# Optimization experiments

Measured on AMD Instinct MI355X. Metric: run time of the kernel, lower is better.

## Reference

```python
import jax, jax.numpy as jnp
import numpy as np

N, C, C2 = 768, 384, 128
H, PQK, PV, CQK, CV = 12, 4, 8, 16, 16
EPS_DIST = 1e-8


def quat_to_rot(q):
    q = q / jnp.linalg.norm(q, axis=-1, keepdims=True)
    w, x, y, z = q[..., 0], q[..., 1], q[..., 2], q[..., 3]
    r0 = jnp.stack([1 - 2 * (y * y + z * z), 2 * (x * y - w * z), 2 * (x * z + w * y)], -1)
    r1 = jnp.stack([2 * (x * y + w * z), 1 - 2 * (x * x + z * z), 2 * (y * z - w * x)], -1)
    r2 = jnp.stack([2 * (x * z - w * y), 2 * (y * z + w * x), 1 - 2 * (x * x + y * y)], -1)
    return jnp.stack([r0, r1, r2], -2)


def layer_norm(x, scale, bias):
    mu = jnp.mean(x, -1, keepdims=True)
    var = jnp.var(x, -1, keepdims=True)
    return (x - mu) * jax.lax.rsqrt(var + 1e-5) * scale + bias


def project_points(x, w, b, rot, trans, p):
    # Linear -> [N,H,3p], split into x/y/z local coords, apply rigid to get global points
    pl = (x @ w + b).reshape(x.shape[0], H, 3 * p)
    loc = jnp.stack(jnp.split(pl, 3, axis=-1), -1)                        # [N,H,p,3]
    return jnp.einsum('nij,nhpj->nhpi', rot, loc) + trans[:, None, None, :]


def setup_inputs() -> dict:
    ks = iter(jax.random.split(jax.random.key(0), 64))
    rn = lambda shape, s: jax.random.normal(next(ks), shape, jnp.float32) * s
    w = lambda shape: rn(shape, 0.02)
    return {
        'inputs_1d': rn([N, C], 1.0),
        'inputs_2d': rn([N, N, C2], 1.0),
        'mask': jnp.ones([N, 1], jnp.float32),
        'rot': quat_to_rot(jax.random.normal(next(ks), [N, 4], jnp.float32)),
        'trans': rn([N, 3], 10.0),
        'w_q_point': w([C, H * 3 * PQK]), 'b_q_point': jnp.zeros([H * 3 * PQK], jnp.float32),
        'w_k_point': w([C, H * 3 * PQK]), 'b_k_point': jnp.zeros([H * 3 * PQK], jnp.float32),
        'w_v_point': w([C, H * 3 * PV]), 'b_v_point': jnp.zeros([H * 3 * PV], jnp.float32),
        'w_q_scalar': w([C, H * CQK]), 'w_k_scalar': w([C, H * CQK]), 'w_v_scalar': w([C, H * CV]),
        'tpw': jnp.full([H], np.log(np.e - 1.0), jnp.float32),
        'w_2d': w([C2, H]), 'b_2d': jnp.zeros([H], jnp.float32),
        'w_out': w([H * CV + 4 * H * PV + H * C2, C]), 'b_out': jnp.zeros([C], jnp.float32),
        'ln1_s': jnp.ones([C], jnp.float32), 'ln1_b': jnp.zeros([C], jnp.float32),
        'w_t1': w([C, C]), 'b_t1': jnp.zeros([C], jnp.float32),
        'w_t2': w([C, C]), 'b_t2': jnp.zeros([C], jnp.float32),
        'w_t3': w([C, C]), 'b_t3': jnp.zeros([C], jnp.float32),
        'ln2_s': jnp.ones([C], jnp.float32), 'ln2_b': jnp.zeros([C], jnp.float32),
        'w_quat': w([C, 6]), 'b_quat': jnp.zeros([6], jnp.float32),
    }


def reference(inputs_1d, inputs_2d, mask, rot, trans,
              w_q_point, b_q_point, w_k_point, b_k_point, w_v_point, b_v_point,
              w_q_scalar, w_k_scalar, w_v_scalar, tpw, w_2d, b_2d, w_out, b_out,
              ln1_s, ln1_b, w_t1, b_t1, w_t2, b_t2, w_t3, b_t3, ln2_s, ln2_b,
              w_quat, b_quat):
    n = inputs_1d.shape[0]
    # ---- Invariant Point Attention ----
    point_w = np.sqrt(2.0 / (9.0 * max(PQK, 1))) * jax.nn.softplus(tpw)   # [H]
    qg = project_points(inputs_1d, w_q_point, b_q_point, rot, trans, PQK)  # [N,H,PQK,3]
    kg = project_points(inputs_1d, w_k_point, b_k_point, rot, trans, PQK)
    # sum_p |q-k|^2 expanded as |q|^2 + |k|^2 - 2 q.k to avoid the [N,N,H,P,3] tensor
    qn = jnp.sum(qg * qg, axis=(-1, -2))                                   # [N,H]
    kn = jnp.sum(kg * kg, axis=(-1, -2))
    cross = jnp.einsum('qhpd,khpd->qkh', qg, kg)
    dist2 = qn[:, None] + kn[None] - 2.0 * cross                           # [N,N,H]
    logits = -0.5 * point_w * dist2
    qs = (inputs_1d @ w_q_scalar).reshape(n, H, CQK) * np.sqrt(1.0 / CQK)
    ksc = (inputs_1d @ w_k_scalar).reshape(n, H, CQK)
    logits += jnp.einsum('qhc,khc->qkh', qs, ksc)
    logits += inputs_2d @ w_2d + b_2d                                      # [N,N,H]
    mask_2d = mask * jnp.swapaxes(mask, -1, -2)                            # [N,N]
    logits -= 1e5 * (1.0 - mask_2d[..., None])
    logits *= np.sqrt(1.0 / 3.0)
    attn = jax.nn.softmax(logits, axis=-2)                                 # softmax over keys
    vs = (inputs_1d @ w_v_scalar).reshape(n, H, CV)
    res_scalar = jnp.einsum('qkh,khc->qhc', attn, vs).reshape(n, -1)
    vg = project_points(inputs_1d, w_v_point, b_v_point, rot, trans, PV)   # [N,H,PV,3]
    rp_g = jnp.einsum('qkh,khpd->qhpd', attn, vg)
    rp_l = jnp.einsum('qdi,qhpd->qhpi', rot, rp_g - trans[:, None, None, :])  # rigid^-1
    norms = jnp.sqrt(jnp.maximum(jnp.sum(rp_l * rp_l, -1), EPS_DIST ** 2))
    res_2d = jnp.einsum('qkh,qkc->qhc', attn, inputs_2d).reshape(n, -1)
    final = jnp.concatenate([
        res_scalar,
        rp_l[..., 0].reshape(n, -1), rp_l[..., 1].reshape(n, -1), rp_l[..., 2].reshape(n, -1),
        norms.reshape(n, -1), res_2d], axis=-1)
    attn_out = final @ w_out + b_out
    # ---- residual + LayerNorm + transition MLP ----
    act = layer_norm(inputs_1d + attn_out, ln1_s, ln1_b)
    x = jax.nn.relu(act @ w_t1 + b_t1)
    x = jax.nn.relu(x @ w_t2 + b_t2)
    x = x @ w_t3 + b_t3
    act = layer_norm(act + x, ln2_s, ln2_b)
    # ---- rigid (quaternion) update: quat = (1, a, b, c), compose with input rigid ----
    v6 = act @ w_quat + b_quat
    quat = jnp.concatenate([jnp.ones_like(v6[:, :1]), v6[:, :3]], -1)
    rot_u = quat_to_rot(quat)
    rot_new = jnp.einsum('nij,njk->nik', rot, rot_u)
    trans_new = jnp.einsum('nij,nj->ni', rot, v6[:, 3:]) + trans
    return jnp.concatenate([act, rot_new.reshape(n, 9), trans_new], axis=-1)
```

## Files before the change

kernel.cpp:

```cpp
#include <hip/hip_runtime.h>


typedef unsigned short bfu;
typedef unsigned int u32;

__device__ __forceinline__ float bf2f(bfu u) {
    return __uint_as_float(((u32)u) << 16);
}
__device__ __forceinline__ bfu f2bf(float f) {
    u32 x = __float_as_uint(f);
    u32 r = x + 0x7fffu + ((x >> 16) & 1u);
    return (bfu)(r >> 16);
}
__device__ __forceinline__ float bflo(u32 u) { return __uint_as_float(u << 16); }
__device__ __forceinline__ float bfhi(u32 u) { return __uint_as_float(u & 0xffff0000u); }

#define OFF_PL      0u
#define OFF_FQ      1769472u
#define OFF_GK      2949120u
#define OFF_VST     4128768u
#define OFF_VGT     4423680u
#define OFF_LOGITS  4866048u
#define OFF_FINAL   33177600u
#define OFF_ATTNOUT 36421632u
#define OFF_ACT     37011456u
#define OFF_X1      37601280u
#define OFF_X2      38191104u
#define OFF_WCAT    38780928u
#define OFF_BCAT    39665664u
#define OFF_CONV    39667968u
#define OFF_FLAG    43684288u

#define CONV_TOTAL 2008158

struct P30 { const void* p[30]; };

static __device__ const int kEnd[30] = {
    294912, 295680, 302592, 304896, 360192, 360336, 415632, 415776,
    526368, 526656, 600384, 674112, 747840, 747852, 749388, 749400,
    1560408, 1560792, 1561176, 1561560, 1709016, 1709400, 1856856, 1857240,
    2004696, 2005080, 2005464, 2005848, 2008152, 2008158
};

__global__ __launch_bounds__(256) void k_convert(P30 ps, bfu* __restrict__ conv,
                                                 u32* __restrict__ flags) {
    u32 pm = *(const u32*)ps.p[1];
    u32 pp = *(const u32*)ps.p[18];
    u32 fA = (pm == 0x3F800000u) ? 1u : 0u;
    u32 fB = (pp == 0x3F800000u) ? 1u : 0u;
    int idx = blockIdx.x * 256 + threadIdx.x;
    if (idx == 0) { flags[0] = fA; flags[1] = fA & fB; }
    if (idx >= CONV_TOTAL) return;
    int t = 0;
    while (idx >= kEnd[t]) ++t;
    int local = idx - (t ? kEnd[t - 1] : 0);
    u32 f = (t < 4) ? fA : fB;
    float v = f ? ((const float*)ps.p[t])[local]
                : bf2f(((const bfu*)ps.p[t])[local]);
    conv[idx] = f2bf(v);
}

__global__ __launch_bounds__(256) void k_concat(
    const bfu* __restrict__ wqs, const bfu* __restrict__ wks, const bfu* __restrict__ wvs,
    const bfu* __restrict__ wqp, const bfu* __restrict__ bqp,
    const bfu* __restrict__ wkp, const bfu* __restrict__ bkp,
    const bfu* __restrict__ wvp, const bfu* __restrict__ bvp,
    bfu* __restrict__ wcat, bfu* __restrict__ bcat) {
    int idx = blockIdx.x * 256 + threadIdx.x;
    if (idx < 384 * 1152) {
        int row = idx / 1152, col = idx - row * 1152;
        bfu v;
        if      (col < 192) v = wqs[row * 192 + col];
        else if (col < 384) v = wks[row * 192 + col - 192];
        else if (col < 576) v = wvs[row * 192 + col - 384];
        else if (col < 720) v = wqp[row * 144 + col - 576];
        else if (col < 864) v = wkp[row * 144 + col - 720];
        else                v = wvp[row * 288 + col - 864];
        wcat[idx] = v;
    } else if (idx < 384 * 1152 + 1152) {
        int col = idx - 384 * 1152;
        bfu v;
        if      (col < 576) v = 0;
        else if (col < 720) v = bqp[col - 576];
        else if (col < 864) v = bkp[col - 720];
        else                v = bvp[col - 864];
        bcat[col] = v;
    }
}

template <int RELU>
__global__ __launch_bounds__(256) void k_gemm(
    const bfu* __restrict__ A, const bfu* __restrict__ W, const bfu* __restrict__ bias,
    bfu* __restrict__ out, int K, int M) {
    __shared__ float As[32][34];
    __shared__ float Ws[32][34];
    int t = threadIdx.x;
    int c0 = blockIdx.x * 32, r0 = blockIdx.y * 32;
    int tr = t >> 4, tc = t & 15;
    float a00 = 0, a01 = 0, a10 = 0, a11 = 0;
    int nch = K >> 5;
    for (int ch = 0; ch < nch; ++ch) {
        int kc = ch * 32;
#pragma unroll
        for (int i = 0; i < 4; ++i) {
            int idx = t + i * 256;
            int r = idx >> 5, c = idx & 31;
            As[c][r] = bf2f(A[(size_t)(r0 + r) * K + kc + c]);
        }
#pragma unroll
        for (int i = 0; i < 4; ++i) {
            int idx = t + i * 256;
            int r = idx >> 5, c = idx & 31;
            Ws[r][c] = bf2f(W[(size_t)(kc + r) * M + c0 + c]);
        }
        __syncthreads();
#pragma unroll
        for (int kk = 0; kk < 32; ++kk) {
            float x0 = As[kk][2 * tr], x1 = As[kk][2 * tr + 1];
            float w0 = Ws[kk][2 * tc], w1 = Ws[kk][2 * tc + 1];
            a00 += x0 * w0; a01 += x0 * w1;
            a10 += x1 * w0; a11 += x1 * w1;
        }
        __syncthreads();
    }
    float b0 = bf2f(bias[c0 + 2 * tc]), b1 = bf2f(bias[c0 + 2 * tc + 1]);
    float v00 = a00 + b0, v01 = a01 + b1, v10 = a10 + b0, v11 = a11 + b1;
    if (RELU) {
        v00 = fmaxf(v00, 0.f); v01 = fmaxf(v01, 0.f);
        v10 = fmaxf(v10, 0.f); v11 = fmaxf(v11, 0.f);
    }
    u32 p0 = (u32)f2bf(v00) | ((u32)f2bf(v01) << 16);
    u32 p1 = (u32)f2bf(v10) | ((u32)f2bf(v11) << 16);
    *(u32*)&out[(size_t)(r0 + 2 * tr) * M + c0 + 2 * tc] = p0;
    *(u32*)&out[(size_t)(r0 + 2 * tr + 1) * M + c0 + 2 * tc] = p1;
}

__global__ __launch_bounds__(64) void k_rigid(
    const bfu* __restrict__ pl, const bfu* __restrict__ rot, const bfu* __restrict__ trans,
    const bfu* __restrict__ tpw, const bfu* __restrict__ b2d,
    float* __restrict__ fq, float* __restrict__ gk,
    bfu* __restrict__ vsT, bfu* __restrict__ vgT) {
    int n = blockIdx.x, t = threadIdx.x;
    __shared__ float pls[1152];
    __shared__ float qgs[144], kgs[144];
    __shared__ float rs[9], ts3[3], pws[12], qns[12], kns[12];
    for (int i = t; i < 1152; i += 64) pls[i] = bf2f(pl[(size_t)n * 1152 + i]);
    if (t < 9)  rs[t] = bf2f(rot[n * 9 + t]);
    if (t < 3)  ts3[t] = bf2f(trans[n * 3 + t]);
    if (t < 12) pws[t] = 0.23570226039551584f * log1pf(expf(bf2f(tpw[t])));
    __syncthreads();
    for (int idx = t; idx < 144; idx += 64) {
        int h = idx / 12, r = idx - h * 12, p = r / 3, i = r - p * 3;
        float q0 = pls[576 + h * 12 + p], q1 = pls[576 + h * 12 + 4 + p], q2 = pls[576 + h * 12 + 8 + p];
        qgs[idx] = rs[i * 3 + 0] * q0 + rs[i * 3 + 1] * q1 + rs[i * 3 + 2] * q2 + ts3[i];
        float k0 = pls[720 + h * 12 + p], k1 = pls[720 + h * 12 + 4 + p], k2 = pls[720 + h * 12 + 8 + p];
        kgs[idx] = rs[i * 3 + 0] * k0 + rs[i * 3 + 1] * k1 + rs[i * 3 + 2] * k2 + ts3[i];
    }
    for (int idx = t; idx < 288; idx += 64) {
        int h = idx / 24, r = idx - h * 24, p = r / 3, i = r - p * 3;
        float v0 = pls[864 + h * 24 + p], v1 = pls[864 + h * 24 + 8 + p], v2 = pls[864 + h * 24 + 16 + p];
        float v = rs[i * 3 + 0] * v0 + rs[i * 3 + 1] * v1 + rs[i * 3 + 2] * v2 + ts3[i];
        vgT[(size_t)idx * 768 + n] = f2bf(v);
    }
    __syncthreads();
    if (t < 12) {
        float s = 0;
        for (int j = 0; j < 12; ++j) s += qgs[t * 12 + j] * qgs[t * 12 + j];
        qns[t] = s;
        s = 0;
        for (int j = 0; j < 12; ++j) s += kgs[t * 12 + j] * kgs[t * 12 + j];
        kns[t] = s;
    }
    __syncthreads();
    for (int idx = t; idx < 12 * 32; idx += 64) {
        int h = idx >> 5, j = idx & 31;
        float fv, gv;
        if (j < 16)      { fv = 0.25f * pls[h * 16 + j];      gv = pls[192 + h * 16 + j]; }
        else if (j < 28) { fv = qgs[h * 12 + j - 16];         gv = pws[h] * kgs[h * 12 + j - 16]; }
        else if (j == 28){ fv = -0.5f * pws[h] * qns[h];      gv = 1.0f; }
        else if (j == 29){ fv = 1.0f;                          gv = -0.5f * pws[h] * kns[h]; }
        else if (j == 30){ fv = bf2f(b2d[h]);                  gv = 1.0f; }
        else             { fv = 0.0f;                          gv = 0.0f; }
        fq[((size_t)n * 12 + h) * 32 + j] = fv;
        gk[((size_t)n * 12 + h) * 32 + j] = gv;
    }
    for (int idx = t; idx < 192; idx += 64)
        vsT[(size_t)idx * 768 + n] = f2bf(pls[384 + idx]);
}

__global__ __launch_bounds__(256) void k2a(
    const float* __restrict__ fq, const float* __restrict__ gk, float* __restrict__ logits) {
    int t = threadIdx.x;
    int k0 = blockIdx.x * 64, q0 = blockIdx.y * 64, h = blockIdx.z;
    __shared__ float Fs[64][33], Gs[64][33];
#pragma unroll
    for (int i = 0; i < 8; ++i) {
        int idx = t + i * 256;
        int r = idx >> 5, c = idx & 31;
        Fs[r][c] = fq[((size_t)(q0 + r) * 12 + h) * 32 + c];
        Gs[r][c] = gk[((size_t)(k0 + r) * 12 + h) * 32 + c];
    }
    __syncthreads();
    int tq = t >> 4, tk = t & 15;
    float acc[4][4] = {};
#pragma unroll
    for (int kk = 0; kk < 32; ++kk) {
        float f0 = Fs[tq * 4 + 0][kk], f1 = Fs[tq * 4 + 1][kk];
        float f2 = Fs[tq * 4 + 2][kk], f3 = Fs[tq * 4 + 3][kk];
        float g0 = Gs[tk * 4 + 0][kk], g1 = Gs[tk * 4 + 1][kk];
        float g2 = Gs[tk * 4 + 2][kk], g3 = Gs[tk * 4 + 3][kk];
        acc[0][0] += f0 * g0; acc[0][1] += f0 * g1; acc[0][2] += f0 * g2; acc[0][3] += f0 * g3;
        acc[1][0] += f1 * g0; acc[1][1] += f1 * g1; acc[1][2] += f1 * g2; acc[1][3] += f1 * g3;
        acc[2][0] += f2 * g0; acc[2][1] += f2 * g1; acc[2][2] += f2 * g2; acc[2][3] += f2 * g3;
        acc[3][0] += f3 * g0; acc[3][1] += f3 * g1; acc[3][2] += f3 * g2; acc[3][3] += f3 * g3;
    }
#pragma unroll
    for (int i = 0; i < 4; ++i) {
        float4 v = make_float4(acc[i][0], acc[i][1], acc[i][2], acc[i][3]);
        *(float4*)&logits[((size_t)h * 768 + q0 + tq * 4 + i) * 768 + k0 + tk * 4] = v;
    }
}

__global__ __launch_bounds__(256) void k2b(
    const void* __restrict__ in2dv, const bfu* __restrict__ w2d,
    const bfu* __restrict__ mask, float* __restrict__ logits,
    const u32* __restrict__ flags) {
    int t = threadIdx.x;
    int q = blockIdx.y, k = blockIdx.x * 256 + t;
    bool f32m = flags[0] != 0u;
    __shared__ __align__(16) float w2ds[12 * 128];
    for (int i = t; i < 1536; i += 256) {
        int cc = i / 12, hh2 = i - cc * 12;
        w2ds[hh2 * 128 + cc] = bf2f(w2d[i]);
    }
    __syncthreads();
    float acc[12] = {};
    size_t base = ((size_t)q * 768 + k) * 128;
    if (f32m) {
        const float4* p = (const float4*)((const float*)in2dv + base);
#pragma unroll 8
        for (int cb = 0; cb < 32; ++cb) {
            float4 u = p[cb];
#pragma unroll
            for (int h = 0; h < 12; ++h) {
                float4 w = *(const float4*)&w2ds[h * 128 + cb * 4];
                acc[h] += u.x * w.x + u.y * w.y + u.z * w.z + u.w * w.w;
            }
        }
    } else {
        const uint2* p = (const uint2*)((const bfu*)in2dv + base);
#pragma unroll 8
        for (int cb = 0; cb < 32; ++cb) {
            uint2 u = p[cb];
            float f0 = bflo(u.x), f1 = bfhi(u.x), f2 = bflo(u.y), f3 = bfhi(u.y);
#pragma unroll
            for (int h = 0; h < 12; ++h) {
                float4 w = *(const float4*)&w2ds[h * 128 + cb * 4];
                acc[h] += f0 * w.x + f1 * w.y + f2 * w.z + f3 * w.w;
            }
        }
    }
    float mq = bf2f(mask[q]), mk = bf2f(mask[k]);
    float mterm = 100000.0f * (1.0f - mq * mk);
#pragma unroll
    for (int h = 0; h < 12; ++h) {
        size_t idx = ((size_t)h * 768 + q) * 768 + k;
        logits[idx] = (logits[idx] + acc[h] - mterm) * 0.5773502691896258f;
    }
}

__global__ __launch_bounds__(256) void k3(
    const float* __restrict__ logits, const void* __restrict__ in2dv,
    const bfu* __restrict__ vsT, const bfu* __restrict__ vgT,
    const bfu* __restrict__ rot, const bfu* __restrict__ trans,
    bfu* __restrict__ finalb, const u32* __restrict__ flags) {
    int q = blockIdx.x, t = threadIdx.x;
    bool f32m = flags[0] != 0u;
    __shared__ __align__(16) float attT[12 * 776];
    __shared__ __align__(16) bfu tile[64 * 128];
    __shared__ float rpg[288];
    __shared__ float rots[9], trs[3];

    for (int h = 0; h < 12; ++h)
        for (int k = t; k < 768; k += 256)
            attT[h * 776 + k] = logits[((size_t)h * 768 + q) * 768 + k];
    __syncthreads();

    if (t < 192) {
        int h = t >> 4, g = t & 15;
        float m = -1e30f;
        for (int i = 0; i < 48; ++i) m = fmaxf(m, attT[h * 776 + g + i * 16]);
#pragma unroll
        for (int off = 1; off < 16; off <<= 1) m = fmaxf(m, __shfl_xor(m, off));
        float s = 0.f;
        for (int i = 0; i < 48; ++i) {
            float v = __expf(attT[h * 776 + g + i * 16] - m);
            attT[h * 776 + g + i * 16] = v;
            s += v;
        }
#pragma unroll
        for (int off = 1; off < 16; off <<= 1) s += __shfl_xor(s, off);
        float rinv = 1.0f / s;
        for (int i = 0; i < 48; ++i) attT[h * 776 + g + i * 16] *= rinv;
    }
    if (t >= 192 && t < 201) rots[t - 192] = bf2f(rot[q * 9 + t - 192]);
    if (t >= 201 && t < 204) trs[t - 201] = bf2f(trans[q * 3 + t - 201]);
    __syncthreads();

    int cp = t & 63, h0 = t >> 6;
    float p00 = 0, p01 = 0, p10 = 0, p11 = 0, p20 = 0, p21 = 0;
    for (int ch = 0; ch < 12; ++ch) {
#pragma unroll
        for (int i = 0; i < 4; ++i) {
            int idx = t + i * 256;
            int r = idx >> 4, g = idx & 15;
            if (f32m) {
                const float* src = (const float*)in2dv +
                    ((size_t)(q * 768 + ch * 64 + r)) * 128 + g * 8;
                float4 a = *(const float4*)src;
                float4 b = *(const float4*)(src + 4);
                uint4 w;
                w.x = (u32)f2bf(a.x) | ((u32)f2bf(a.y) << 16);
                w.y = (u32)f2bf(a.z) | ((u32)f2bf(a.w) << 16);
                w.z = (u32)f2bf(b.x) | ((u32)f2bf(b.y) << 16);
                w.w = (u32)f2bf(b.z) | ((u32)f2bf(b.w) << 16);
                ((uint4*)tile)[idx] = w;
            } else {
                ((uint4*)tile)[idx] = *(const uint4*)((const bfu*)in2dv +
                    ((size_t)(q * 768 + ch * 64 + r)) * 128 + g * 8);
            }
        }
        __syncthreads();
        const u32* tp = (const u32*)tile;
        const float4* a0p = (const float4*)&attT[(h0 + 0) * 776 + ch * 64];
        const float4* a1p = (const float4*)&attT[(h0 + 4) * 776 + ch * 64];
        const float4* a2p = (const float4*)&attT[(h0 + 8) * 776 + ch * 64];
#pragma unroll 4
        for (int k4 = 0; k4 < 16; ++k4) {
            float4 a0 = a0p[k4], a1 = a1p[k4], a2 = a2p[k4];
            float a0v[4] = {a0.x, a0.y, a0.z, a0.w};
            float a1v[4] = {a1.x, a1.y, a1.z, a1.w};
            float a2v[4] = {a2.x, a2.y, a2.z, a2.w};
#pragma unroll
            for (int u = 0; u < 4; ++u) {
                u32 uu = tp[(k4 * 4 + u) * 64 + cp];
                float lo = bflo(uu), hi = bfhi(uu);
                p00 += a0v[u] * lo; p01 += a0v[u] * hi;
                p10 += a1v[u] * lo; p11 += a1v[u] * hi;
                p20 += a2v[u] * lo; p21 += a2v[u] * hi;
            }
        }
        __syncthreads();
    }
    {
        bfu* fb = finalb + (size_t)q * 2112 + 576;
        *(u32*)&fb[(h0 + 0) * 128 + 2 * cp] = (u32)f2bf(p00) | ((u32)f2bf(p01) << 16);
        *(u32*)&fb[(h0 + 4) * 128 + 2 * cp] = (u32)f2bf(p10) | ((u32)f2bf(p11) << 16);
        *(u32*)&fb[(h0 + 8) * 128 + 2 * cp] = (u32)f2bf(p20) | ((u32)f2bf(p21) << 16);
    }

    if (t < 120) {
        int h = t / 10, oi = t - h * 10;
        const bfu* rp[4];
#pragma unroll
        for (int j = 0; j < 4; ++j) {
            int o = oi * 4 + j;
            rp[j] = (o < 16) ? (vsT + (size_t)(h * 16 + o) * 768)
                             : (vgT + (size_t)(h * 24 + o - 16) * 768);
        }
        float acc[4] = {};
        for (int kb = 0; kb < 96; ++kb) {
            int k8 = kb * 8;
            float4 aL = *(const float4*)&attT[h * 776 + k8];
            float4 aH = *(const float4*)&attT[h * 776 + k8 + 4];
#pragma unroll
            for (int j = 0; j < 4; ++j) {
                uint4 u = *(const uint4*)(rp[j] + k8);
                acc[j] += aL.x * bflo(u.x) + aL.y * bfhi(u.x)
                        + aL.z * bflo(u.y) + aL.w * bfhi(u.y)
                        + aH.x * bflo(u.z) + aH.y * bfhi(u.z)
                        + aH.z * bflo(u.w) + aH.w * bfhi(u.w);
            }
        }
#pragma unroll
        for (int j = 0; j < 4; ++j) {
            int o = oi * 4 + j;
            if (o < 16) finalb[(size_t)q * 2112 + h * 16 + o] = f2bf(acc[j]);
            else rpg[h * 24 + o - 16] = acc[j];
        }
    }
    __syncthreads();

    if (t < 96) {
        int h = t >> 3, p = t & 7;
        float v0 = rpg[h * 24 + p * 3 + 0] - trs[0];
        float v1 = rpg[h * 24 + p * 3 + 1] - trs[1];
        float v2 = rpg[h * 24 + p * 3 + 2] - trs[2];
        float r0 = rots[0] * v0 + rots[3] * v1 + rots[6] * v2;
        float r1 = rots[1] * v0 + rots[4] * v1 + rots[7] * v2;
        float r2 = rots[2] * v0 + rots[5] * v1 + rots[8] * v2;
        float nn = sqrtf(fmaxf(r0 * r0 + r1 * r1 + r2 * r2, 1e-16f));
        size_t fb = (size_t)q * 2112;
        finalb[fb + 192 + h * 8 + p] = f2bf(r0);
        finalb[fb + 288 + h * 8 + p] = f2bf(r1);
        finalb[fb + 384 + h * 8 + p] = f2bf(r2);
        finalb[fb + 480 + h * 8 + p] = f2bf(nn);
    }
}

__global__ __launch_bounds__(128) void k_ln(
    const bfu* __restrict__ a, const bfu* __restrict__ b,
    const bfu* __restrict__ sc, const bfu* __restrict__ bi,
    bfu* __restrict__ outb, void* __restrict__ outf, const u32* __restrict__ flags) {
    int r = blockIdx.x, t = threadIdx.x;
    __shared__ float red[2][2];
    float x[3];
    float s = 0.f, ss = 0.f;
#pragma unroll
    for (int i = 0; i < 3; ++i) {
        int c = t + i * 128;
        float v = bf2f(a[(size_t)r * 384 + c]) + bf2f(b[(size_t)r * 384 + c]);
        x[i] = v; s += v; ss += v * v;
    }
#pragma unroll
    for (int off = 1; off < 64; off <<= 1) { s += __shfl_xor(s, off); ss += __shfl_xor(ss, off); }
    int w = t >> 6;
    if ((t & 63) == 0) { red[w][0] = s; red[w][1] = ss; }
    __syncthreads();
    s = red[0][0] + red[1][0];
    ss = red[0][1] + red[1][1];
    float mu = s * (1.0f / 384.0f);
    float var = ss * (1.0f / 384.0f) - mu * mu;
    float rstd = rsqrtf(var + 1e-5f);
    bool f32o = flags[1] != 0u;
#pragma unroll
    for (int i = 0; i < 3; ++i) {
        int c = t + i * 128;
        float v = (x[i] - mu) * rstd * bf2f(sc[c]) + bf2f(bi[c]);
        outb[(size_t)r * 384 + c] = f2bf(v);
        if (outf) {
            if (f32o) ((float*)outf)[(size_t)r * 396 + c] = v;
            else      ((bfu*)outf)[(size_t)r * 396 + c] = f2bf(v);
        }
    }
}

__global__ __launch_bounds__(64) void k_quat(
    const bfu* __restrict__ act2,
    const bfu* __restrict__ rot, const bfu* __restrict__ trans,
    const bfu* __restrict__ wq, const bfu* __restrict__ bq,
    void* __restrict__ doutv, const u32* __restrict__ flags) {
    int r = blockIdx.x, t = threadIdx.x;
    float acc[6] = {};
    for (int i = 0; i < 6; ++i) {
        int k = t + i * 64;
        float xv = bf2f(act2[(size_t)r * 384 + k]);
#pragma unroll
        for (int o = 0; o < 6; ++o) acc[o] += xv * bf2f(wq[k * 6 + o]);
    }
#pragma unroll
    for (int o = 0; o < 6; ++o) {
#pragma unroll
        for (int off = 1; off < 64; off <<= 1) acc[o] += __shfl_xor(acc[o], off);
    }
    if (t == 0) {
        bool f32o = flags[1] != 0u;
        float v[6];
        for (int o = 0; o < 6; ++o) v[o] = acc[o] + bf2f(bq[o]);
        float w_ = 1.0f, x_ = v[0], y_ = v[1], z_ = v[2];
        float inv = rsqrtf(w_ * w_ + x_ * x_ + y_ * y_ + z_ * z_);
        w_ *= inv; x_ *= inv; y_ *= inv; z_ *= inv;
        float U[9];
        U[0] = 1 - 2 * (y_ * y_ + z_ * z_); U[1] = 2 * (x_ * y_ - w_ * z_); U[2] = 2 * (x_ * z_ + w_ * y_);
        U[3] = 2 * (x_ * y_ + w_ * z_); U[4] = 1 - 2 * (x_ * x_ + z_ * z_); U[5] = 2 * (y_ * z_ - w_ * x_);
        U[6] = 2 * (x_ * z_ - w_ * y_); U[7] = 2 * (y_ * z_ + w_ * x_); U[8] = 1 - 2 * (x_ * x_ + y_ * y_);
        float R[9];
        for (int i = 0; i < 9; ++i) R[i] = bf2f(rot[r * 9 + i]);
        for (int i = 0; i < 3; ++i)
            for (int j = 0; j < 3; ++j) {
                float sum = R[i * 3] * U[j] + R[i * 3 + 1] * U[3 + j] + R[i * 3 + 2] * U[6 + j];
                if (f32o) ((float*)doutv)[(size_t)r * 396 + 384 + i * 3 + j] = sum;
                else      ((bfu*)doutv)[(size_t)r * 396 + 384 + i * 3 + j] = f2bf(sum);
            }
        for (int i = 0; i < 3; ++i) {
            float sum = R[i * 3] * v[3] + R[i * 3 + 1] * v[4] + R[i * 3 + 2] * v[5] + bf2f(trans[r * 3 + i]);
            if (f32o) ((float*)doutv)[(size_t)r * 396 + 393 + i] = sum;
            else      ((bfu*)doutv)[(size_t)r * 396 + 393 + i] = f2bf(sum);
        }
    }
}

extern "C" void kernel_launch(void* const* d_in, const int* in_sizes, int n_in,
                              void* d_out, int out_size, void* d_ws, size_t ws_size,
                              hipStream_t stream) {
    (void)in_sizes; (void)n_in; (void)out_size; (void)ws_size;

    char* ws = (char*)d_ws;
    bfu* pl      = (bfu*)(ws + OFF_PL);
    float* fq    = (float*)(ws + OFF_FQ);
    float* gk    = (float*)(ws + OFF_GK);
    bfu* vsT     = (bfu*)(ws + OFF_VST);
    bfu* vgT     = (bfu*)(ws + OFF_VGT);
    float* logit = (float*)(ws + OFF_LOGITS);
    bfu* finalb  = (bfu*)(ws + OFF_FINAL);
    bfu* attnout = (bfu*)(ws + OFF_ATTNOUT);
    bfu* act     = (bfu*)(ws + OFF_ACT);
    bfu* x1      = (bfu*)(ws + OFF_X1);
    bfu* x2      = (bfu*)(ws + OFF_X2);
    bfu* act2    = x2;
    bfu* wcat    = (bfu*)(ws + OFF_WCAT);
    bfu* bcat    = (bfu*)(ws + OFF_BCAT);
    bfu* conv    = (bfu*)(ws + OFF_CONV);
    u32* flags   = (u32*)(ws + OFF_FLAG);

    static const int offs[30] = {
        0, 294912, 295680, 302592, 304896, 360192, 360336, 415632, 415776,
        526368, 526656, 600384, 674112, 747840, 747852, 749388, 749400,
        1560408, 1560792, 1561176, 1561560, 1709016, 1709400, 1856856, 1857240,
        2004696, 2005080, 2005464, 2005848, 2008152
    };
    const bfu* c_in1d = conv + offs[0];
    const bfu* c_mask = conv + offs[1];
    const bfu* c_rot  = conv + offs[2];
    const bfu* c_trns = conv + offs[3];
    const bfu* c_wqp  = conv + offs[4];
    const bfu* c_bqp  = conv + offs[5];
    const bfu* c_wkp  = conv + offs[6];
    const bfu* c_bkp  = conv + offs[7];
    const bfu* c_wvp  = conv + offs[8];
    const bfu* c_bvp  = conv + offs[9];
    const bfu* c_wqs  = conv + offs[10];
    const bfu* c_wks  = conv + offs[11];
    const bfu* c_wvs  = conv + offs[12];
    const bfu* c_tpw  = conv + offs[13];
    const bfu* c_w2d  = conv + offs[14];
    const bfu* c_b2d  = conv + offs[15];
    const bfu* c_wout = conv + offs[16];
    const bfu* c_bout = conv + offs[17];
    const bfu* c_ln1s = conv + offs[18];
    const bfu* c_ln1b = conv + offs[19];
    const bfu* c_wt1  = conv + offs[20];
    const bfu* c_bt1  = conv + offs[21];
    const bfu* c_wt2  = conv + offs[22];
    const bfu* c_bt2  = conv + offs[23];
    const bfu* c_wt3  = conv + offs[24];
    const bfu* c_bt3  = conv + offs[25];
    const bfu* c_ln2s = conv + offs[26];
    const bfu* c_ln2b = conv + offs[27];
    const bfu* c_wqt  = conv + offs[28];
    const bfu* c_bqt  = conv + offs[29];

    P30 ps;
    ps.p[0] = d_in[0];
    for (int i = 1; i < 30; ++i) ps.p[i] = d_in[i + 1];
    const void* in2d = d_in[1];

    k_convert<<<(CONV_TOTAL + 255) / 256, 256, 0, stream>>>(ps, conv, flags);
    k_concat<<<1733, 256, 0, stream>>>(c_wqs, c_wks, c_wvs, c_wqp, c_bqp, c_wkp, c_bkp,
                                       c_wvp, c_bvp, wcat, bcat);
    k_gemm<0><<<dim3(36, 24), 256, 0, stream>>>(c_in1d, wcat, bcat, pl, 384, 1152);
    k_rigid<<<768, 64, 0, stream>>>(pl, c_rot, c_trns, c_tpw, c_b2d, fq, gk, vsT, vgT);
    k2a<<<dim3(12, 12, 12), 256, 0, stream>>>(fq, gk, logit);
    k2b<<<dim3(3, 768), 256, 0, stream>>>(in2d, c_w2d, c_mask, logit, flags);
    k3<<<768, 256, 0, stream>>>(logit, in2d, vsT, vgT, c_rot, c_trns, finalb, flags);
    k_gemm<0><<<dim3(12, 24), 256, 0, stream>>>(finalb, c_wout, c_bout, attnout, 2112, 384);
    k_ln<<<768, 128, 0, stream>>>(c_in1d, attnout, c_ln1s, c_ln1b, act, nullptr, flags);
    k_gemm<1><<<dim3(12, 24), 256, 0, stream>>>(act, c_wt1, c_bt1, x1, 384, 384);
    k_gemm<1><<<dim3(12, 24), 256, 0, stream>>>(x1, c_wt2, c_bt2, x2, 384, 384);
    k_gemm<0><<<dim3(12, 24), 256, 0, stream>>>(x2, c_wt3, c_bt3, x1, 384, 384);
    k_ln<<<768, 128, 0, stream>>>(act, x1, c_ln2s, c_ln2b, act2, d_out, flags);
    k_quat<<<768, 64, 0, stream>>>(act2, c_rot, c_trns, c_wqt, c_bqt, d_out, flags);
}
```

Before: 955.8 us.

## Fuse logits, pair bias and softmax per query; retile GEMMs to 64x64

Replaces the separate logits GEMM, pair-bias pass and softmax with one per-query kernel. It computes the point and scalar logits from a transposed key-feature buffer, adds the 2D bias, applies softmax in shared memory and writes normalized attention. The aggregation kernel now streams inputs_2d directly without a staged shared tile and splits value work across more threads. The GEMMs move to 64x64 tiles with 4x4 register blocking and packed loads. Together this removes a logits round trip and several launches, at the cost of strided per-key global reads in the fused kernel and lower GEMM block counts.

```diff
diff --git a/kernel.cpp b/kernel.cpp
--- a/kernel.cpp
+++ b/kernel.cpp
@@ -17,10 +17,10 @@
 
 #define OFF_PL      0u
 #define OFF_FQ      1769472u
-#define OFF_GK      2949120u
+#define OFF_GKT     2949120u
 #define OFF_VST     4128768u
 #define OFF_VGT     4423680u
-#define OFF_LOGITS  4866048u
+#define OFF_ATTN    4866048u
 #define OFF_FINAL   33177600u
 #define OFF_ATTNOUT 36421632u
 #define OFF_ACT     37011456u
@@ -89,56 +89,65 @@
 }
 
 template <int RELU>
-__global__ __launch_bounds__(256) void k_gemm(
+__global__ __launch_bounds__(256) void k_gemm64(
     const bfu* __restrict__ A, const bfu* __restrict__ W, const bfu* __restrict__ bias,
     bfu* __restrict__ out, int K, int M) {
-    __shared__ float As[32][34];
-    __shared__ float Ws[32][34];
+    __shared__ float As[32][69];
+    __shared__ float Ws[32][69];
     int t = threadIdx.x;
-    int c0 = blockIdx.x * 32, r0 = blockIdx.y * 32;
+    int c0 = blockIdx.x * 64, r0 = blockIdx.y * 64;
     int tr = t >> 4, tc = t & 15;
-    float a00 = 0, a01 = 0, a10 = 0, a11 = 0;
-    int nch = K >> 5;
-    for (int ch = 0; ch < nch; ++ch) {
-        int kc = ch * 32;
+    float acc[4][4] = {};
+    for (int kc = 0; kc < K; kc += 32) {
 #pragma unroll
         for (int i = 0; i < 4; ++i) {
             int idx = t + i * 256;
-            int r = idx >> 5, c = idx & 31;
-            As[c][r] = bf2f(A[(size_t)(r0 + r) * K + kc + c]);
+            int r = idx >> 4, c2 = idx & 15;
+            u32 u = *(const u32*)&A[(size_t)(r0 + r) * K + kc + 2 * c2];
+            As[2 * c2][r] = bflo(u); As[2 * c2 + 1][r] = bfhi(u);
         }
 #pragma unroll
         for (int i = 0; i < 4; ++i) {
             int idx = t + i * 256;
-            int r = idx >> 5, c = idx & 31;
-            Ws[r][c] = bf2f(W[(size_t)(kc + r) * M + c0 + c]);
+            int r = idx >> 5, c2 = idx & 31;
+            u32 u = *(const u32*)&W[(size_t)(kc + r) * M + c0 + 2 * c2];
+            Ws[r][2 * c2] = bflo(u); Ws[r][2 * c2 + 1] = bfhi(u);
         }
         __syncthreads();
 #pragma unroll
         for (int kk = 0; kk < 32; ++kk) {
-            float x0 = As[kk][2 * tr], x1 = As[kk][2 * tr + 1];
-            float w0 = Ws[kk][2 * tc], w1 = Ws[kk][2 * tc + 1];
-            a00 += x0 * w0; a01 += x0 * w1;
-            a10 += x1 * w0; a11 += x1 * w1;
+            float x[4], w[4];
+#pragma unroll
+            for (int j = 0; j < 4; ++j) { x[j] = As[kk][4 * tr + j]; w[j] = Ws[kk][4 * tc + j]; }
+#pragma unroll
+            for (int a = 0; a < 4; ++a)
+#pragma unroll
+                for (int b = 0; b < 4; ++b) acc[a][b] += x[a] * w[b];
         }
         __syncthreads();
     }
-    float b0 = bf2f(bias[c0 + 2 * tc]), b1 = bf2f(bias[c0 + 2 * tc + 1]);
-    float v00 = a00 + b0, v01 = a01 + b1, v10 = a10 + b0, v11 = a11 + b1;
-    if (RELU) {
-        v00 = fmaxf(v00, 0.f); v01 = fmaxf(v01, 0.f);
-        v10 = fmaxf(v10, 0.f); v11 = fmaxf(v11, 0.f);
-    }
-    u32 p0 = (u32)f2bf(v00) | ((u32)f2bf(v01) << 16);
-    u32 p1 = (u32)f2bf(v10) | ((u32)f2bf(v11) << 16);
-    *(u32*)&out[(size_t)(r0 + 2 * tr) * M + c0 + 2 * tc] = p0;
-    *(u32*)&out[(size_t)(r0 + 2 * tr + 1) * M + c0 + 2 * tc] = p1;
+    float bv[4];
+#pragma unroll
+    for (int b = 0; b < 4; ++b) bv[b] = bf2f(bias[c0 + 4 * tc + b]);
+#pragma unroll
+    for (int a = 0; a < 4; ++a) {
+        float v[4];
+#pragma unroll
+        for (int b = 0; b < 4; ++b) {
+            v[b] = acc[a][b] + bv[b];
+            if (RELU) v[b] = fmaxf(v[b], 0.f);
+        }
+        uint2 pk;
+        pk.x = (u32)f2bf(v[0]) | ((u32)f2bf(v[1]) << 16);
+        pk.y = (u32)f2bf(v[2]) | ((u32)f2bf(v[3]) << 16);
+        *(uint2*)&out[(size_t)(r0 + 4 * tr + a) * M + c0 + 4 * tc] = pk;
+    }
 }
 
 __global__ __launch_bounds__(64) void k_rigid(
     const bfu* __restrict__ pl, const bfu* __restrict__ rot, const bfu* __restrict__ trans,
     const bfu* __restrict__ tpw, const bfu* __restrict__ b2d,
-    float* __restrict__ fq, float* __restrict__ gk,
+    float* __restrict__ fq, float* __restrict__ gkT,
     bfu* __restrict__ vsT, bfu* __restrict__ vgT) {
     int n = blockIdx.x, t = threadIdx.x;
     __shared__ float pls[1152];
@@ -181,176 +190,141 @@
         else if (j == 29){ fv = 1.0f;                          gv = -0.5f * pws[h] * kns[h]; }
         else if (j == 30){ fv = bf2f(b2d[h]);                  gv = 1.0f; }
         else             { fv = 0.0f;                          gv = 0.0f; }
-        fq[((size_t)n * 12 + h) * 32 + j] = fv;
-        gk[((size_t)n * 12 + h) * 32 + j] = gv;
+        fq[(size_t)n * 384 + idx] = fv;
+        gkT[(size_t)idx * 768 + n] = gv;
     }
     for (int idx = t; idx < 192; idx += 64)
         vsT[(size_t)idx * 768 + n] = f2bf(pls[384 + idx]);
 }
 
-__global__ __launch_bounds__(256) void k2a(
-    const float* __restrict__ fq, const float* __restrict__ gk, float* __restrict__ logits) {
-    int t = threadIdx.x;
-    int k0 = blockIdx.x * 64, q0 = blockIdx.y * 64, h = blockIdx.z;
-    __shared__ float Fs[64][33], Gs[64][33];
-#pragma unroll
-    for (int i = 0; i < 8; ++i) {
-        int idx = t + i * 256;
-        int r = idx >> 5, c = idx & 31;
-        Fs[r][c] = fq[((size_t)(q0 + r) * 12 + h) * 32 + c];
-        Gs[r][c] = gk[((size_t)(k0 + r) * 12 + h) * 32 + c];
-    }
-    __syncthreads();
-    int tq = t >> 4, tk = t & 15;
-    float acc[4][4] = {};
-#pragma unroll
-    for (int kk = 0; kk < 32; ++kk) {
-        float f0 = Fs[tq * 4 + 0][kk], f1 = Fs[tq * 4 + 1][kk];
-        float f2 = Fs[tq * 4 + 2][kk], f3 = Fs[tq * 4 + 3][kk];
-        float g0 = Gs[tk * 4 + 0][kk], g1 = Gs[tk * 4 + 1][kk];
-        float g2 = Gs[tk * 4 + 2][kk], g3 = Gs[tk * 4 + 3][kk];
-        acc[0][0] += f0 * g0; acc[0][1] += f0 * g1; acc[0][2] += f0 * g2; acc[0][3] += f0 * g3;
-        acc[1][0] += f1 * g0; acc[1][1] += f1 * g1; acc[1][2] += f1 * g2; acc[1][3] += f1 * g3;
-        acc[2][0] += f2 * g0; acc[2][1] += f2 * g1; acc[2][2] += f2 * g2; acc[2][3] += f2 * g3;
-        acc[3][0] += f3 * g0; acc[3][1] += f3 * g1; acc[3][2] += f3 * g2; acc[3][3] += f3 * g3;
-    }
-#pragma unroll
-    for (int i = 0; i < 4; ++i) {
-        float4 v = make_float4(acc[i][0], acc[i][1], acc[i][2], acc[i][3]);
-        *(float4*)&logits[((size_t)h * 768 + q0 + tq * 4 + i) * 768 + k0 + tk * 4] = v;
-    }
-}
-
-__global__ __launch_bounds__(256) void k2b(
+__global__ __launch_bounds__(256) void k_fused(
+    const float* __restrict__ fq, const float* __restrict__ gkT,
     const void* __restrict__ in2dv, const bfu* __restrict__ w2d,
-    const bfu* __restrict__ mask, float* __restrict__ logits,
+    const bfu* __restrict__ mask, float* __restrict__ attn,
     const u32* __restrict__ flags) {
-    int t = threadIdx.x;
-    int q = blockIdx.y, k = blockIdx.x * 256 + t;
+    int q = blockIdx.x, t = threadIdx.x;
     bool f32m = flags[0] != 0u;
+    __shared__ float lg[12 * 776];
     __shared__ __align__(16) float w2ds[12 * 128];
+    __shared__ __align__(16) float fqs[384];
     for (int i = t; i < 1536; i += 256) {
-        int cc = i / 12, hh2 = i - cc * 12;
-        w2ds[hh2 * 128 + cc] = bf2f(w2d[i]);
-    }
-    __syncthreads();
-    float acc[12] = {};
-    size_t base = ((size_t)q * 768 + k) * 128;
-    if (f32m) {
-        const float4* p = (const float4*)((const float*)in2dv + base);
+        int cc = i / 12, hh = i - cc * 12;
+        w2ds[hh * 128 + cc] = bf2f(w2d[i]);
+    }
+    for (int i = t; i < 384; i += 256) fqs[i] = fq[(size_t)q * 384 + i];
+    float mq = bf2f(mask[q]);
+    __syncthreads();
+
+    for (int ch = 0; ch < 3; ++ch) {
+        int k = ch * 256 + t;
+        float acc[12] = {};
+        size_t base = ((size_t)q * 768 + k) * 128;
+        if (f32m) {
+            const float4* p = (const float4*)((const float*)in2dv + base);
 #pragma unroll 8
-        for (int cb = 0; cb < 32; ++cb) {
-            float4 u = p[cb];
-#pragma unroll
-            for (int h = 0; h < 12; ++h) {
-                float4 w = *(const float4*)&w2ds[h * 128 + cb * 4];
-                acc[h] += u.x * w.x + u.y * w.y + u.z * w.z + u.w * w.w;
+            for (int cb = 0; cb < 32; ++cb) {
+                float4 u = p[cb];
+#pragma unroll
+                for (int h = 0; h < 12; ++h) {
+                    float4 w = *(const float4*)&w2ds[h * 128 + cb * 4];
+                    acc[h] += u.x * w.x + u.y * w.y + u.z * w.z + u.w * w.w;
+                }
             }
-        }
-    } else {
-        const uint2* p = (const uint2*)((const bfu*)in2dv + base);
+        } else {
+            const uint2* p = (const uint2*)((const bfu*)in2dv + base);
 #pragma unroll 8
-        for (int cb = 0; cb < 32; ++cb) {
-            uint2 u = p[cb];
-            float f0 = bflo(u.x), f1 = bfhi(u.x), f2 = bflo(u.y), f3 = bfhi(u.y);
-#pragma unroll
-            for (int h = 0; h < 12; ++h) {
-                float4 w = *(const float4*)&w2ds[h * 128 + cb * 4];
-                acc[h] += f0 * w.x + f1 * w.y + f2 * w.z + f3 * w.w;
+            for (int cb = 0; cb < 32; ++cb) {
+                uint2 u = p[cb];
+                float f0 = bflo(u.x), f1 = bfhi(u.x), f2 = bflo(u.y), f3 = bfhi(u.y);
+#pragma unroll
+                for (int h = 0; h < 12; ++h) {
+                    float4 w = *(const float4*)&w2ds[h * 128 + cb * 4];
+                    acc[h] += f0 * w.x + f1 * w.y + f2 * w.z + f3 * w.w;
+                }
             }
         }
-    }
-    float mq = bf2f(mask[q]), mk = bf2f(mask[k]);
-    float mterm = 100000.0f * (1.0f - mq * mk);
-#pragma unroll
-    for (int h = 0; h < 12; ++h) {
-        size_t idx = ((size_t)h * 768 + q) * 768 + k;
-        logits[idx] = (logits[idx] + acc[h] - mterm) * 0.5773502691896258f;
-    }
-}
-
-__global__ __launch_bounds__(256) void k3(
-    const float* __restrict__ logits, const void* __restrict__ in2dv,
+        float mk = bf2f(mask[k]);
+        float mterm = 100000.0f * (1.0f - mq * mk);
+#pragma unroll 1
+        for (int h = 0; h < 12; ++h) {
+            float s = 0.f;
+            const float* g = gkT + (size_t)(h * 32) * 768 + k;
+            const float* f = fqs + h * 32;
+#pragma unroll 8
+            for (int c = 0; c < 32; ++c) s += g[(size_t)c * 768] * f[c];
+            lg[h * 776 + k] = (s + acc[h] - mterm) * 0.5773502691896258f;
+        }
+    }
+    __syncthreads();
+
+    if (t < 192) {
+        int h = t >> 4, g = t & 15;
+        float m = -1e30f;
+        for (int i = 0; i < 48; ++i) m = fmaxf(m, lg[h * 776 + g + i * 16]);
+#pragma unroll
+        for (int off = 1; off < 16; off <<= 1) m = fmaxf(m, __shfl_xor(m, off));
+        float s = 0.f;
+        for (int i = 0; i < 48; ++i) {
+            float v = __expf(lg[h * 776 + g + i * 16] - m);
+            lg[h * 776 + g + i * 16] = v;
+            s += v;
+        }
+#pragma unroll
+        for (int off = 1; off < 16; off <<= 1) s += __shfl_xor(s, off);
+        float rinv = 1.0f / s;
+        for (int i = 0; i < 48; ++i) lg[h * 776 + g + i * 16] *= rinv;
+    }
+    __syncthreads();
+    for (int h = 0; h < 12; ++h)
+        for (int k = t; k < 768; k += 256)
+            attn[(size_t)q * 9216 + h * 768 + k] = lg[h * 776 + k];
+}
+
+__global__ __launch_bounds__(256) void k3b(
+    const float* __restrict__ attn, const void* __restrict__ in2dv,
     const bfu* __restrict__ vsT, const bfu* __restrict__ vgT,
     const bfu* __restrict__ rot, const bfu* __restrict__ trans,
     bfu* __restrict__ finalb, const u32* __restrict__ flags) {
     int q = blockIdx.x, t = threadIdx.x;
     bool f32m = flags[0] != 0u;
-    __shared__ __align__(16) float attT[12 * 776];
-    __shared__ __align__(16) bfu tile[64 * 128];
+    __shared__ __align__(16) float lgs[12 * 776];
     __shared__ float rpg[288];
     __shared__ float rots[9], trs[3];
 
     for (int h = 0; h < 12; ++h)
         for (int k = t; k < 768; k += 256)
-            attT[h * 776 + k] = logits[((size_t)h * 768 + q) * 768 + k];
-    __syncthreads();
-
-    if (t < 192) {
-        int h = t >> 4, g = t & 15;
-        float m = -1e30f;
-        for (int i = 0; i < 48; ++i) m = fmaxf(m, attT[h * 776 + g + i * 16]);
-#pragma unroll
-        for (int off = 1; off < 16; off <<= 1) m = fmaxf(m, __shfl_xor(m, off));
-        float s = 0.f;
-        for (int i = 0; i < 48; ++i) {
-            float v = __expf(attT[h * 776 + g + i * 16] - m);
-            attT[h * 776 + g + i * 16] = v;
-            s += v;
-        }
-#pragma unroll
-        for (int off = 1; off < 16; off <<= 1) s += __shfl_xor(s, off);
-        float rinv = 1.0f / s;
-        for (int i = 0; i < 48; ++i) attT[h * 776 + g + i * 16] *= rinv;
-    }
-    if (t >= 192 && t < 201) rots[t - 192] = bf2f(rot[q * 9 + t - 192]);
-    if (t >= 201 && t < 204) trs[t - 201] = bf2f(trans[q * 3 + t - 201]);
+            lgs[h * 776 + k] = attn[(size_t)q * 9216 + h * 768 + k];
+    if (t < 9)  rots[t] = bf2f(rot[q * 9 + t]);
+    if (t >= 16 && t < 19) trs[t - 16] = bf2f(trans[q * 3 + t - 16]);
     __syncthreads();
 
     int cp = t & 63, h0 = t >> 6;
     float p00 = 0, p01 = 0, p10 = 0, p11 = 0, p20 = 0, p21 = 0;
-    for (int ch = 0; ch < 12; ++ch) {
-#pragma unroll
-        for (int i = 0; i < 4; ++i) {
-            int idx = t + i * 256;
-            int r = idx >> 4, g = idx & 15;
-            if (f32m) {
-                const float* src = (const float*)in2dv +
-                    ((size_t)(q * 768 + ch * 64 + r)) * 128 + g * 8;
-                float4 a = *(const float4*)src;
-                float4 b = *(const float4*)(src + 4);
-                uint4 w;
-                w.x = (u32)f2bf(a.x) | ((u32)f2bf(a.y) << 16);
-                w.y = (u32)f2bf(a.z) | ((u32)f2bf(a.w) << 16);
-                w.z = (u32)f2bf(b.x) | ((u32)f2bf(b.y) << 16);
-                w.w = (u32)f2bf(b.z) | ((u32)f2bf(b.w) << 16);
-                ((uint4*)tile)[idx] = w;
-            } else {
-                ((uint4*)tile)[idx] = *(const uint4*)((const bfu*)in2dv +
-                    ((size_t)(q * 768 + ch * 64 + r)) * 128 + g * 8);
-            }
-        }
-        __syncthreads();
-        const u32* tp = (const u32*)tile;
-        const float4* a0p = (const float4*)&attT[(h0 + 0) * 776 + ch * 64];
-        const float4* a1p = (const float4*)&attT[(h0 + 4) * 776 + ch * 64];
-        const float4* a2p = (const float4*)&attT[(h0 + 8) * 776 + ch * 64];
+    if (f32m) {
+        const float2* p2 = (const float2*)((const float*)in2dv + (size_t)q * 98304) + cp;
 #pragma unroll 4
-        for (int k4 = 0; k4 < 16; ++k4) {
-            float4 a0 = a0p[k4], a1 = a1p[k4], a2 = a2p[k4];
-            float a0v[4] = {a0.x, a0.y, a0.z, a0.w};
-            float a1v[4] = {a1.x, a1.y, a1.z, a1.w};
-            float a2v[4] = {a2.x, a2.y, a2.z, a2.w};
-#pragma unroll
-            for (int u = 0; u < 4; ++u) {
-                u32 uu = tp[(k4 * 4 + u) * 64 + cp];
-                float lo = bflo(uu), hi = bfhi(uu);
-                p00 += a0v[u] * lo; p01 += a0v[u] * hi;
-                p10 += a1v[u] * lo; p11 += a1v[u] * hi;
-                p20 += a2v[u] * lo; p21 += a2v[u] * hi;
-            }
-        }
-        __syncthreads();
+        for (int k = 0; k < 768; ++k) {
+            float2 v = p2[(size_t)k * 64];
+            float a0 = lgs[(h0 + 0) * 776 + k];
+            float a1 = lgs[(h0 + 4) * 776 + k];
+            float a2 = lgs[(h0 + 8) * 776 + k];
+            p00 += a0 * v.x; p01 += a0 * v.y;
+            p10 += a1 * v.x; p11 += a1 * v.y;
+            p20 += a2 * v.x; p21 += a2 * v.y;
+        }
+    } else {
+        const u32* pu = (const u32*)in2dv + (size_t)q * 49152 + cp;
+#pragma unroll 4
+        for (int k = 0; k < 768; ++k) {
+            u32 u = pu[(size_t)k * 64];
+            float vx = bflo(u), vy = bfhi(u);
+            float a0 = lgs[(h0 + 0) * 776 + k];
+            float a1 = lgs[(h0 + 4) * 776 + k];
+            float a2 = lgs[(h0 + 8) * 776 + k];
+            p00 += a0 * vx; p01 += a0 * vy;
+            p10 += a1 * vx; p11 += a1 * vy;
+            p20 += a2 * vx; p21 += a2 * vy;
+        }
     }
     {
         bfu* fb = finalb + (size_t)q * 2112 + 576;
@@ -359,35 +333,33 @@
         *(u32*)&fb[(h0 + 8) * 128 + 2 * cp] = (u32)f2bf(p20) | ((u32)f2bf(p21) << 16);
     }
 
-    if (t < 120) {
-        int h = t / 10, oi = t - h * 10;
-        const bfu* rp[4];
-#pragma unroll
-        for (int j = 0; j < 4; ++j) {
-            int o = oi * 4 + j;
-            rp[j] = (o < 16) ? (vsT + (size_t)(h * 16 + o) * 768)
-                             : (vgT + (size_t)(h * 24 + o - 16) * 768);
-        }
-        float acc[4] = {};
+    if (t < 240) {
+        int o0 = 2 * t;
+        int h = o0 / 40, r0 = o0 - h * 40, r1 = r0 + 1;
+        const bfu* rowA = (r0 < 16) ? (vsT + (size_t)(h * 16 + r0) * 768)
+                                    : (vgT + (size_t)(h * 24 + r0 - 16) * 768);
+        const bfu* rowB = (r1 < 16) ? (vsT + (size_t)(h * 16 + r1) * 768)
+                                    : (vgT + (size_t)(h * 24 + r1 - 16) * 768);
+        float aA = 0.f, aB = 0.f;
         for (int kb = 0; kb < 96; ++kb) {
             int k8 = kb * 8;
-            float4 aL = *(const float4*)&attT[h * 776 + k8];
-            float4 aH = *(const float4*)&attT[h * 776 + k8 + 4];
-#pragma unroll
-            for (int j = 0; j < 4; ++j) {
-                uint4 u = *(const uint4*)(rp[j] + k8);
-                acc[j] += aL.x * bflo(u.x) + aL.y * bfhi(u.x)
-                        + aL.z * bflo(u.y) + aL.w * bfhi(u.y)
-                        + aH.x * bflo(u.z) + aH.y * bfhi(u.z)
-                        + aH.z * bflo(u.w) + aH.w * bfhi(u.w);
-            }
-        }
-#pragma unroll
-        for (int j = 0; j < 4; ++j) {
-            int o = oi * 4 + j;
-            if (o < 16) finalb[(size_t)q * 2112 + h * 16 + o] = f2bf(acc[j]);
-            else rpg[h * 24 + o - 16] = acc[j];
-        }
+            float4 aL = *(const float4*)&lgs[h * 776 + k8];
+            float4 aH = *(const float4*)&lgs[h * 776 + k8 + 4];
+            uint4 uA = *(const uint4*)(rowA + k8);
+            uint4 uB = *(const uint4*)(rowB + k8);
+            aA += aL.x * bflo(uA.x) + aL.y * bfhi(uA.x)
+                + aL.z * bflo(uA.y) + aL.w * bfhi(uA.y)
+                + aH.x * bflo(uA.z) + aH.y * bfhi(uA.z)
+                + aH.z * bflo(uA.w) + aH.w * bfhi(uA.w);
+            aB += aL.x * bflo(uB.x) + aL.y * bfhi(uB.x)
+                + aL.z * bflo(uB.y) + aL.w * bfhi(uB.y)
+                + aH.x * bflo(uB.z) + aH.y * bfhi(uB.z)
+                + aH.z * bflo(uB.w) + aH.w * bfhi(uB.w);
+        }
+        if (r0 < 16) finalb[(size_t)q * 2112 + h * 16 + r0] = f2bf(aA);
+        else rpg[h * 24 + r0 - 16] = aA;
+        if (r1 < 16) finalb[(size_t)q * 2112 + h * 16 + r1] = f2bf(aB);
+        else rpg[h * 24 + r1 - 16] = aB;
     }
     __syncthreads();
 
@@ -498,10 +470,10 @@
     char* ws = (char*)d_ws;
     bfu* pl      = (bfu*)(ws + OFF_PL);
     float* fq    = (float*)(ws + OFF_FQ);
-    float* gk    = (float*)(ws + OFF_GK);
+    float* gkT   = (float*)(ws + OFF_GKT);
     bfu* vsT     = (bfu*)(ws + OFF_VST);
     bfu* vgT     = (bfu*)(ws + OFF_VGT);
-    float* logit = (float*)(ws + OFF_LOGITS);
+    float* attn  = (float*)(ws + OFF_ATTN);
     bfu* finalb  = (bfu*)(ws + OFF_FINAL);
     bfu* attnout = (bfu*)(ws + OFF_ATTNOUT);
     bfu* act     = (bfu*)(ws + OFF_ACT);
@@ -558,16 +530,15 @@
     k_convert<<<(CONV_TOTAL + 255) / 256, 256, 0, stream>>>(ps, conv, flags);
     k_concat<<<1733, 256, 0, stream>>>(c_wqs, c_wks, c_wvs, c_wqp, c_bqp, c_wkp, c_bkp,
                                        c_wvp, c_bvp, wcat, bcat);
-    k_gemm<0><<<dim3(36, 24), 256, 0, stream>>>(c_in1d, wcat, bcat, pl, 384, 1152);
-    k_rigid<<<768, 64, 0, stream>>>(pl, c_rot, c_trns, c_tpw, c_b2d, fq, gk, vsT, vgT);
-    k2a<<<dim3(12, 12, 12), 256, 0, stream>>>(fq, gk, logit);
-    k2b<<<dim3(3, 768), 256, 0, stream>>>(in2d, c_w2d, c_mask, logit, flags);
-    k3<<<768, 256, 0, stream>>>(logit, in2d, vsT, vgT, c_rot, c_trns, finalb, flags);
-    k_gemm<0><<<dim3(12, 24), 256, 0, stream>>>(finalb, c_wout, c_bout, attnout, 2112, 384);
+    k_gemm64<0><<<dim3(18, 12), 256, 0, stream>>>(c_in1d, wcat, bcat, pl, 384, 1152);
+    k_rigid<<<768, 64, 0, stream>>>(pl, c_rot, c_trns, c_tpw, c_b2d, fq, gkT, vsT, vgT);
+    k_fused<<<768, 256, 0, stream>>>(fq, gkT, in2d, c_w2d, c_mask, attn, flags);
+    k3b<<<768, 256, 0, stream>>>(attn, in2d, vsT, vgT, c_rot, c_trns, finalb, flags);
+    k_gemm64<0><<<dim3(6, 12), 256, 0, stream>>>(finalb, c_wout, c_bout, attnout, 2112, 384);
     k_ln<<<768, 128, 0, stream>>>(c_in1d, attnout, c_ln1s, c_ln1b, act, nullptr, flags);
-    k_gemm<1><<<dim3(12, 24), 256, 0, stream>>>(act, c_wt1, c_bt1, x1, 384, 384);
-    k_gemm<1><<<dim3(12, 24), 256, 0, stream>>>(x1, c_wt2, c_bt2, x2, 384, 384);
-    k_gemm<0><<<dim3(12, 24), 256, 0, stream>>>(x2, c_wt3, c_bt3, x1, 384, 384);
+    k_gemm64<1><<<dim3(6, 12), 256, 0, stream>>>(act, c_wt1, c_bt1, x1, 384, 384);
+    k_gemm64<1><<<dim3(6, 12), 256, 0, stream>>>(x1, c_wt2, c_bt2, x2, 384, 384);
+    k_gemm64<0><<<dim3(6, 12), 256, 0, stream>>>(x2, c_wt3, c_bt3, x1, 384, 384);
     k_ln<<<768, 128, 0, stream>>>(act, x1, c_ln2s, c_ln2b, act2, d_out, flags);
     k_quat<<<768, 64, 0, stream>>>(act2, c_rot, c_trns, c_wqt, c_bqt, d_out, flags);
 }
```

Result: slower. 994.1 us (+4.0%).
